# Optimization experiments

Measured on AMD Instinct MI355X. Metric: run time of the kernel, lower is better.

Reference implementation:

```python
import jax, jax.numpy as jnp
import numpy as np

C = 256
D = C // 8  # 32


def setup_inputs() -> dict:
    key = jax.random.key(0)
    ks = jax.random.split(key, 9)
    B, H, W = 4, 64, 64
    x = jax.random.normal(ks[0], (B, C, H, W), dtype=jnp.float32)
    # 1x1 conv weights stored as [out, in] matrices (kernel_size=1)
    s = 1.0 / np.sqrt(C)
    Wf = jax.random.uniform(ks[1], (D, C), jnp.float32, -s, s)
    Wg = jax.random.uniform(ks[2], (D, C), jnp.float32, -s, s)
    Wh = jax.random.uniform(ks[3], (D, C), jnp.float32, -s, s)
    sv = 1.0 / np.sqrt(D)
    Wv = jax.random.uniform(ks[4], (C, D), jnp.float32, -sv, sv)
    bf = jnp.zeros((D,), jnp.float32)
    bg = jnp.zeros((D,), jnp.float32)
    bh = jnp.zeros((D,), jnp.float32)
    bv = jax.random.uniform(ks[5], (C,), jnp.float32, -sv, sv)
    # gamma initialized to zero in the module; use a nonzero value so output is non-trivial
    gamma = jnp.array([0.5], jnp.float32)
    return {"x": x, "Wf": Wf, "bf": bf, "Wg": Wg, "bg": bg,
            "Wh": Wh, "bh": bh, "Wv": Wv, "bv": bv, "gamma": gamma}


def reference(x, Wf, bf, Wg, bg, Wh, bh, Wv, bv, gamma):
    B, Cc, Hh, Ww = x.shape
    N = Hh * Ww
    xf = x.reshape(B, Cc, N)  # flatten spatial tokens, [B, C, N]
    # 1x1 convs == channel matmuls
    f = jnp.einsum('dc,bcn->bdn', Wf, xf) + bf[None, :, None]  # [B, D, N]
    g = jnp.einsum('dc,bcn->bdn', Wg, xf) + bg[None, :, None]
    h = jnp.einsum('dc,bcn->bdn', Wh, xf) + bh[None, :, None]
    # unscaled attention: f^T g -> [B, N, N], softmax over last axis
    attn = jax.nn.softmax(jnp.einsum('bdn,bdm->bnm', f, g), axis=-1)
    # h @ attn: out[:, d, m] = sum_n h[:, d, n] * attn[:, n, m]
    sa = jnp.einsum('bdn,bnm->bdm', h, attn)  # [B, D, N]
    # output 1x1 conv D -> C
    o = jnp.einsum('cd,bdn->bcn', Wv, sa) + bv[None, :, None]
    out = gamma[0] * o.reshape(B, Cc, Hh, Ww)
    return out
```

## Files before the change

### kernel.cpp

```cpp
#include <hip/hip_runtime.h>

typedef __bf16 bf16;
typedef bf16 bf16x4 __attribute__((ext_vector_type(4)));
typedef bf16 bf16x8 __attribute__((ext_vector_type(8)));
typedef float f32x4 __attribute__((ext_vector_type(4)));

#define NB 4
#define NC 256
#define ND 32
#define NN 4096
#define NSPLIT 8
#define MSPLIT 8
#define CSPL 8

__global__ __launch_bounds__(256) void k_wcvt(
    const float* __restrict__ Wf, const float* __restrict__ Wg,
    const float* __restrict__ Wh, bf16* __restrict__ Wstk)
{
    int e0 = (blockIdx.x * 256 + threadIdx.x) * 8;
    int row = e0 >> 8;
    int tensor = row >> 5;
    const float* src = tensor == 0 ? Wf : tensor == 1 ? Wg : Wh;
    const float* sp = src + (row & 31) * NC + (e0 & 255);
    bf16x8 v;
    #pragma unroll
    for (int j = 0; j < 8; ++j) v[j] = (bf16)sp[j];
    *reinterpret_cast<bf16x8*>(Wstk + e0) = v;
}

__global__ __launch_bounds__(512) void k_fgh(
    const float* __restrict__ x,
    const bf16* __restrict__ Wstk,
    const float* __restrict__ bfp, const float* __restrict__ bgp,
    const float* __restrict__ bhp,
    bf16* __restrict__ fT, bf16* __restrict__ gT, bf16* __restrict__ hM)
{
    __shared__ __align__(16) char xb[64 * 512];
    const int b  = blockIdx.y;
    const int n0 = blockIdx.x * 64;
    const int t  = threadIdx.x;
    const int lane = t & 63;
    const int w  = t >> 6;
    const int l15 = lane & 15;
    const int l4  = lane >> 4;

    {
        const int nl  = t & 63;
        const int swz = (nl & 7) << 4;
        const int chi = (t >> 6) * 8;
        #pragma unroll
        for (int pass = 0; pass < 4; ++pass) {
            int c0 = pass * 64 + chi;
            const float* xp = x + ((size_t)b * NC + c0) * NN + n0 + nl;
            bf16x8 v;
            #pragma unroll
            for (int j = 0; j < 8; ++j) v[j] = (bf16)xp[(size_t)j * NN];
            *reinterpret_cast<bf16x8*>(&xb[nl * 512 + ((c0 * 2) ^ swz)]) = v;
        }
    }
    __syncthreads();

    const int ncol = (w & 3) * 16 + l15;
    const int nswz = (ncol & 7) << 4;
    const int n    = n0 + ncol;
    const int dsub = l4 * 4;
    const int rtb  = (w >> 2) * 3;

    #pragma unroll
    for (int rr = 0; rr < 3; ++rr) {
        int rt = rtb + rr;
        int tensor = rt >> 1;
        int d0 = (rt & 1) * 16;
        f32x4 acc = {0.f, 0.f, 0.f, 0.f};
        #pragma unroll
        for (int kc = 0; kc < 8; ++kc) {
            bf16x8 a = *reinterpret_cast<const bf16x8*>(
                Wstk + (rt * 16 + l15) * NC + kc * 32 + l4 * 8);
            bf16x8 bb = *reinterpret_cast<const bf16x8*>(
                &xb[ncol * 512 + ((kc * 64 + l4 * 16) ^ nswz)]);
            acc = __builtin_amdgcn_mfma_f32_16x16x32_bf16(a, bb, acc, 0, 0, 0);
        }
        const float* bsel = tensor == 0 ? bfp : tensor == 1 ? bgp : bhp;
        int dbase = d0 + dsub;
        if (tensor < 2) {
            bf16x4 vv;
            #pragma unroll
            for (int r = 0; r < 4; ++r) vv[r] = (bf16)(acc[r] + bsel[dbase + r]);
            bf16* dst = (tensor == 0 ? fT : gT) + ((size_t)b * NN + n) * ND + dbase;
            *reinterpret_cast<bf16x4*>(dst) = vv;
        } else {
            #pragma unroll
            for (int r = 0; r < 4; ++r)
                hM[((size_t)b * ND + dbase + r) * NN + n] =
                    (bf16)(acc[r] + bsel[dbase + r]);
        }
    }
}

__global__ __launch_bounds__(256) void k_rowsum(
    const bf16* __restrict__ fT, const bf16* __restrict__ gT,
    float* __restrict__ Lpart)
{
    const int b  = blockIdx.z;
    const int ms = blockIdx.y;
    const int nb = blockIdx.x * 64;
    const int t  = threadIdx.x;
    const int lane = t & 63;
    const int w  = t >> 6;
    const int l15 = lane & 15;
    const int l4  = lane >> 4;

    bf16x8 a = *reinterpret_cast<const bf16x8*>(
        fT + ((size_t)b * NN + nb + w * 16 + l15) * ND + l4 * 8);
    float sum0 = 0.f, sum1 = 0.f, sum2 = 0.f, sum3 = 0.f;
    const bf16* gp = gT + (size_t)b * NN * ND
                   + ((size_t)ms * (NN / MSPLIT) + l15) * ND + l4 * 8;
    #pragma unroll 4
    for (int m = 0; m < NN / MSPLIT; m += 32) {
        bf16x8 b0 = *reinterpret_cast<const bf16x8*>(gp + (size_t)m * ND);
        bf16x8 b1 = *reinterpret_cast<const bf16x8*>(gp + (size_t)(m + 16) * ND);
        f32x4 z = {0.f, 0.f, 0.f, 0.f};
        f32x4 s0 = __builtin_amdgcn_mfma_f32_16x16x32_bf16(a, b0, z, 0, 0, 0);
        f32x4 s1 = __builtin_amdgcn_mfma_f32_16x16x32_bf16(a, b1, z, 0, 0, 0);
        sum0 += __expf(s0[0]) + __expf(s1[0]);
        sum1 += __expf(s0[1]) + __expf(s1[1]);
        sum2 += __expf(s0[2]) + __expf(s1[2]);
        sum3 += __expf(s0[3]) + __expf(s1[3]);
    }
    float sv[4] = {sum0, sum1, sum2, sum3};
    #pragma unroll
    for (int r = 0; r < 4; ++r) {
        float v = sv[r];
        v += __shfl_xor(v, 1);
        v += __shfl_xor(v, 2);
        v += __shfl_xor(v, 4);
        v += __shfl_xor(v, 8);
        sv[r] = v;
    }
    if (l15 == 0) {
        #pragma unroll
        for (int r = 0; r < 4; ++r)
            Lpart[((size_t)ms * NB + b) * NN + nb + w * 16 + l4 * 4 + r] = sv[r];
    }
}

__global__ __launch_bounds__(256) void k_attn(
    const bf16* __restrict__ fT, const bf16* __restrict__ gT,
    const bf16* __restrict__ hM, const float* __restrict__ Lpart,
    float* __restrict__ saWS)
{
    __shared__ __align__(16) char fL[64 * 80];
    __shared__ __align__(16) char hL[32 * 144];
    __shared__ __align__(16) char Pl[4 * 2048];
    __shared__ float rlL[64];

    const int b  = blockIdx.z;
    const int ns = blockIdx.y;
    const int m0 = blockIdx.x * 64;
    const int t  = threadIdx.x;
    const int lane = t & 63;
    const int w  = t >> 6;
    const int l15 = lane & 15;
    const int l4  = lane >> 4;

    bf16x8 gfrag = *reinterpret_cast<const bf16x8*>(
        gT + ((size_t)b * NN + m0 + w * 16 + l15) * ND + l4 * 8);

    f32x4 acc0 = {0.f, 0.f, 0.f, 0.f};
    f32x4 acc1 = {0.f, 0.f, 0.f, 0.f};

    char* Pw = &Pl[w * 2048];
    const int mswz = (l15 & 7) << 4;

    const int s_nl = t >> 2;
    const int s_dl = (t & 3) * 8;
    const int s_d  = t >> 3;
    const int s_ne = (t & 7) * 8;
    const bf16* fsrc = fT + (size_t)b * NN * ND;
    const bf16* hsrc = hM + (size_t)b * ND * NN;

    const int nbeg = ns * (NN / NSPLIT);
    const int nend = nbeg + NN / NSPLIT;

    for (int n1 = nbeg; n1 < nend; n1 += 64) {
        __syncthreads();
        *reinterpret_cast<bf16x8*>(&fL[s_nl * 80 + s_dl * 2]) =
            *reinterpret_cast<const bf16x8*>(fsrc + (size_t)(n1 + s_nl) * ND + s_dl);
        *reinterpret_cast<bf16x8*>(&hL[s_d * 144 + s_ne * 2]) =
            *reinterpret_cast<const bf16x8*>(hsrc + (size_t)s_d * NN + n1 + s_ne);
        if (t < 64) {
            float s = 0.f;
            #pragma unroll
            for (int ms = 0; ms < MSPLIT; ++ms)
                s += Lpart[((size_t)ms * NB + b) * NN + n1 + t];
            rlL[t] = 1.0f / s;
        }
        __syncthreads();

        #pragma unroll
        for (int nt = 0; nt < 4; ++nt) {
            bf16x8 afrag = *reinterpret_cast<const bf16x8*>(
                &fL[(nt * 16 + l15) * 80 + l4 * 16]);
            f32x4 z = {0.f, 0.f, 0.f, 0.f};
            f32x4 s = __builtin_amdgcn_mfma_f32_16x16x32_bf16(afrag, gfrag, z, 0, 0, 0);
            bf16x4 p4;
            #pragma unroll
            for (int r = 0; r < 4; ++r)
                p4[r] = (bf16)(__expf(s[r]) * rlL[nt * 16 + l4 * 4 + r]);
            *reinterpret_cast<bf16x4*>(
                &Pw[l15 * 128 + ((nt * 32 + l4 * 8) ^ mswz)]) = p4;
        }
        #pragma unroll
        for (int kc = 0; kc < 2; ++kc) {
            bf16x8 pb = *reinterpret_cast<const bf16x8*>(
                &Pw[l15 * 128 + ((kc * 64 + l4 * 16) ^ mswz)]);
            bf16x8 h0 = *reinterpret_cast<const bf16x8*>(
                &hL[l15 * 144 + kc * 64 + l4 * 16]);
            acc0 = __builtin_amdgcn_mfma_f32_16x16x32_bf16(h0, pb, acc0, 0, 0, 0);
            bf16x8 h1 = *reinterpret_cast<const bf16x8*>(
                &hL[(16 + l15) * 144 + kc * 64 + l4 * 16]);
            acc1 = __builtin_amdgcn_mfma_f32_16x16x32_bf16(h1, pb, acc1, 0, 0, 0);
        }
    }

    float* sp = saWS + (((size_t)ns * NB + b) * NN + m0 + w * 16 + l15) * ND;
    *reinterpret_cast<f32x4*>(sp + l4 * 4)      = acc0;
    *reinterpret_cast<f32x4*>(sp + 16 + l4 * 4) = acc1;
}

__global__ __launch_bounds__(256) void k_proj(
    const float* __restrict__ saWS,
    const float* __restrict__ Wv, const float* __restrict__ bv,
    const float* __restrict__ gamma, float* __restrict__ out)
{
    __shared__ float sa_s[64 * 33];
    const int b  = blockIdx.z;
    const int c0 = blockIdx.y * (NC / CSPL);
    const int m0 = blockIdx.x * 64;
    const int t  = threadIdx.x;

    #pragma unroll
    for (int p = t; p < 64 * 8; p += 256) {
        int m = p >> 3, dq = (p & 7) * 4;
        float s0 = 0.f, s1 = 0.f, s2 = 0.f, s3 = 0.f;
        #pragma unroll
        for (int s4 = 0; s4 < NSPLIT; ++s4) {
            f32x4 v = *reinterpret_cast<const f32x4*>(
                saWS + (((size_t)s4 * NB + b) * NN + m0 + m) * ND + dq);
            s0 += v[0]; s1 += v[1]; s2 += v[2]; s3 += v[3];
        }
        float* dp = &sa_s[m * 33 + dq];
        dp[0] = s0; dp[1] = s1; dp[2] = s2; dp[3] = s3;
    }
    __syncthreads();

    const int mloc = t & 63;
    const int cg   = t >> 6;
    float sav[32];
    #pragma unroll
    for (int d = 0; d < 32; ++d) sav[d] = sa_s[mloc * 33 + d];
    const float g0 = gamma[0];
    float* op = out + (size_t)b * NC * NN + m0 + mloc;
    #pragma unroll
    for (int i = 0; i < 8; ++i) {
        int c = c0 + cg * 8 + i;
        const float* wp = Wv + c * ND;
        float sum = bv[c];
        #pragma unroll
        for (int d = 0; d < 32; ++d) sum = fmaf(wp[d], sav[d], sum);
        op[(size_t)c * NN] = g0 * sum;
    }
}

extern "C" void kernel_launch(void* const* d_in, const int* in_sizes, int n_in,
                              void* d_out, int out_size, void* d_ws, size_t ws_size,
                              hipStream_t stream)
{
    const float* x   = (const float*)d_in[0];
    const float* Wf  = (const float*)d_in[1];
    const float* bfp = (const float*)d_in[2];
    const float* Wg  = (const float*)d_in[3];
    const float* bgp = (const float*)d_in[4];
    const float* Wh  = (const float*)d_in[5];
    const float* bhp = (const float*)d_in[6];
    const float* Wv  = (const float*)d_in[7];
    const float* bv  = (const float*)d_in[8];
    const float* gm  = (const float*)d_in[9];
    float* out = (float*)d_out;

    char* ws = (char*)d_ws;
    bf16*  Wstk  = (bf16*)ws;
    bf16*  fT    = (bf16*)(ws + 49152);
    bf16*  gT    = (bf16*)(ws + 49152 + (1u << 20));
    bf16*  hM    = (bf16*)(ws + 49152 + (2u << 20));
    float* Lpart = (float*)(ws + 49152 + (3u << 20));
    float* saWS  = (float*)(ws + 49152 + (3u << 20) + (512u << 10));

    k_wcvt  <<<dim3(12),              dim3(256), 0, stream>>>(Wf, Wg, Wh, Wstk);
    k_fgh   <<<dim3(64, NB),          dim3(512), 0, stream>>>(x, Wstk, bfp, bgp, bhp, fT, gT, hM);
    k_rowsum<<<dim3(64, MSPLIT, NB),  dim3(256), 0, stream>>>(fT, gT, Lpart);
    k_attn  <<<dim3(64, NSPLIT, NB),  dim3(256), 0, stream>>>(fT, gT, hM, Lpart, saWS);
    k_proj  <<<dim3(64, CSPL, NB),    dim3(256), 0, stream>>>(saWS, Wv, bv, gm, out);
}
```

Baseline: 157.3 us.

## Fuse all stages into one cooperative persistent kernel with grid syncs

Replaces the five separate launches with one cooperative kernel of 512 blocks that loops over virtual work units. Stages are separated by grid-wide barriers: projection of f/g/h (weights now converted inline), row sums, attention, and output projection. The split factors drop from 8 to 4, so each block does more work per unit and there are fewer partial sums to reduce. This removes launch gaps and the weight-conversion kernel, at the cost of grid.sync overhead and fewer parallel blocks per stage. The old multi-kernel path remains as a fallback if the cooperative launch fails.

```diff
diff --git a/kernel.cpp b/kernel.cpp
--- a/kernel.cpp
+++ b/kernel.cpp
@@ -1,4 +1,7 @@
 #include <hip/hip_runtime.h>
+#include <hip/hip_cooperative_groups.h>
+
+namespace cg = cooperative_groups;
 
 typedef __bf16 bf16;
 typedef bf16 bf16x4 __attribute__((ext_vector_type(4)));
@@ -9,9 +12,268 @@
 #define NC 256
 #define ND 32
 #define NN 4096
-#define NSPLIT 8
-#define MSPLIT 8
-#define CSPL 8
+#define SPL 4
+#define GRID 512
+#define VUNITS 2
+
+__global__ __launch_bounds__(256, 2) void k_mega(
+    const float* __restrict__ x,
+    const float* __restrict__ Wf, const float* __restrict__ bfp,
+    const float* __restrict__ Wg, const float* __restrict__ bgp,
+    const float* __restrict__ Wh, const float* __restrict__ bhp,
+    const float* __restrict__ Wv, const float* __restrict__ bv,
+    const float* __restrict__ gamma,
+    bf16* __restrict__ fT, bf16* __restrict__ gT, bf16* __restrict__ hM,
+    float* __restrict__ Lpart, float* __restrict__ saWS,
+    float* __restrict__ out)
+{
+    __shared__ __align__(16) char smem[18432];
+    cg::grid_group grid = cg::this_grid();
+
+    const int bid  = blockIdx.x;
+    const int t    = threadIdx.x;
+    const int lane = t & 63;
+    const int w    = t >> 6;
+    const int l15  = lane & 15;
+    const int l4   = lane >> 4;
+
+    for (int u = 0; u < VUNITS; ++u) {
+        __syncthreads();
+        const int vbid = (u << 9) | bid;
+        const int b    = vbid >> 8;
+        const int rest = vbid & 255;
+        const int n0   = (rest >> 1) * 32;
+        const int half = rest & 1;
+        char* xb = smem;
+
+        {
+            const int nl  = t & 31;
+            const int swz = (nl & 7) << 4;
+            const int chi = (t >> 5) * 8;
+            #pragma unroll
+            for (int pass = 0; pass < 4; ++pass) {
+                int c0 = pass * 64 + chi;
+                const float* xp = x + ((size_t)b * NC + c0) * NN + n0 + nl;
+                bf16x8 v;
+                #pragma unroll
+                for (int j = 0; j < 8; ++j) v[j] = (bf16)xp[(size_t)j * NN];
+                *reinterpret_cast<bf16x8*>(&xb[nl * 512 + ((c0 * 2) ^ swz)]) = v;
+            }
+        }
+        __syncthreads();
+
+        #pragma unroll
+        for (int rep = 0; rep < 2; ++rep) {
+            int tk = w + 4 * rep;
+            if (tk < 6) {
+                const int strip  = tk & 1;
+                const int rt     = half * 3 + (tk >> 1);
+                const int tensor = rt >> 1;
+                const float* Wsel = tensor == 0 ? Wf : tensor == 1 ? Wg : Wh;
+                const float* bsel = tensor == 0 ? bfp : tensor == 1 ? bgp : bhp;
+                const int drow = (rt & 1) * 16 + l15;
+                const int ncol = strip * 16 + l15;
+                const int nswz = (ncol & 7) << 4;
+                f32x4 acc = {0.f, 0.f, 0.f, 0.f};
+                #pragma unroll
+                for (int kc = 0; kc < 8; ++kc) {
+                    const float* wp = Wsel + drow * NC + kc * 32 + l4 * 8;
+                    f32x4 wlo = *reinterpret_cast<const f32x4*>(wp);
+                    f32x4 whi = *reinterpret_cast<const f32x4*>(wp + 4);
+                    bf16x8 a;
+                    #pragma unroll
+                    for (int j = 0; j < 4; ++j) {
+                        a[j]     = (bf16)wlo[j];
+                        a[4 + j] = (bf16)whi[j];
+                    }
+                    bf16x8 bb = *reinterpret_cast<const bf16x8*>(
+                        &xb[ncol * 512 + ((kc * 64 + l4 * 16) ^ nswz)]);
+                    acc = __builtin_amdgcn_mfma_f32_16x16x32_bf16(a, bb, acc, 0, 0, 0);
+                }
+                const int dbase = (rt & 1) * 16 + l4 * 4;
+                const int n = n0 + ncol;
+                if (tensor < 2) {
+                    bf16x4 vv;
+                    #pragma unroll
+                    for (int r = 0; r < 4; ++r) vv[r] = (bf16)(acc[r] + bsel[dbase + r]);
+                    bf16* dst = (tensor == 0 ? fT : gT) + ((size_t)b * NN + n) * ND + dbase;
+                    *reinterpret_cast<bf16x4*>(dst) = vv;
+                } else {
+                    #pragma unroll
+                    for (int r = 0; r < 4; ++r)
+                        hM[((size_t)b * ND + dbase + r) * NN + n] =
+                            (bf16)(acc[r] + bsel[dbase + r]);
+                }
+            }
+        }
+    }
+    __threadfence();
+    grid.sync();
+
+    for (int u = 0; u < VUNITS; ++u) {
+        const int vbid = (u << 9) | bid;
+        const int b  = vbid >> 8;
+        const int r_ = vbid & 255;
+        const int nb = (r_ >> 2) * 64;
+        const int ms = r_ & 3;
+
+        bf16x8 a = *reinterpret_cast<const bf16x8*>(
+            fT + ((size_t)b * NN + nb + w * 16 + l15) * ND + l4 * 8);
+        float sum0 = 0.f, sum1 = 0.f, sum2 = 0.f, sum3 = 0.f;
+        const bf16* gp = gT + (size_t)b * NN * ND
+                       + ((size_t)ms * (NN / SPL) + l15) * ND + l4 * 8;
+        #pragma unroll 4
+        for (int m = 0; m < NN / SPL; m += 32) {
+            bf16x8 b0 = *reinterpret_cast<const bf16x8*>(gp + (size_t)m * ND);
+            bf16x8 b1 = *reinterpret_cast<const bf16x8*>(gp + (size_t)(m + 16) * ND);
+            f32x4 z = {0.f, 0.f, 0.f, 0.f};
+            f32x4 s0 = __builtin_amdgcn_mfma_f32_16x16x32_bf16(a, b0, z, 0, 0, 0);
+            f32x4 s1 = __builtin_amdgcn_mfma_f32_16x16x32_bf16(a, b1, z, 0, 0, 0);
+            sum0 += __expf(s0[0]) + __expf(s1[0]);
+            sum1 += __expf(s0[1]) + __expf(s1[1]);
+            sum2 += __expf(s0[2]) + __expf(s1[2]);
+            sum3 += __expf(s0[3]) + __expf(s1[3]);
+        }
+        float sv[4] = {sum0, sum1, sum2, sum3};
+        #pragma unroll
+        for (int r = 0; r < 4; ++r) {
+            float v = sv[r];
+            v += __shfl_xor(v, 1);
+            v += __shfl_xor(v, 2);
+            v += __shfl_xor(v, 4);
+            v += __shfl_xor(v, 8);
+            sv[r] = v;
+        }
+        if (l15 == 0) {
+            #pragma unroll
+            for (int r = 0; r < 4; ++r)
+                Lpart[((size_t)ms * NB + b) * NN + nb + w * 16 + l4 * 4 + r] = sv[r];
+        }
+    }
+    __threadfence();
+    grid.sync();
+
+    for (int u = 0; u < VUNITS; ++u) {
+        char* fL  = smem;
+        char* hL  = smem + 5120;
+        char* Pl  = smem + 9728;
+        float* rlL = (float*)(smem + 17920);
+
+        const int vbid = (u << 9) | bid;
+        const int b  = vbid >> 8;
+        const int r_ = vbid & 255;
+        const int m0 = (r_ >> 2) * 64;
+        const int ns = r_ & 3;
+
+        bf16x8 gfrag = *reinterpret_cast<const bf16x8*>(
+            gT + ((size_t)b * NN + m0 + w * 16 + l15) * ND + l4 * 8);
+
+        f32x4 acc0 = {0.f, 0.f, 0.f, 0.f};
+        f32x4 acc1 = {0.f, 0.f, 0.f, 0.f};
+
+        char* Pw = &Pl[w * 2048];
+        const int mswz = (l15 & 7) << 4;
+
+        const int s_nl = t >> 2;
+        const int s_dl = (t & 3) * 8;
+        const int s_d  = t >> 3;
+        const int s_ne = (t & 7) * 8;
+        const bf16* fsrc = fT + (size_t)b * NN * ND;
+        const bf16* hsrc = hM + (size_t)b * ND * NN;
+
+        const int nbeg = ns * (NN / SPL);
+        const int nend = nbeg + NN / SPL;
+
+        for (int n1 = nbeg; n1 < nend; n1 += 64) {
+            __syncthreads();
+            *reinterpret_cast<bf16x8*>(&fL[s_nl * 80 + s_dl * 2]) =
+                *reinterpret_cast<const bf16x8*>(fsrc + (size_t)(n1 + s_nl) * ND + s_dl);
+            *reinterpret_cast<bf16x8*>(&hL[s_d * 144 + s_ne * 2]) =
+                *reinterpret_cast<const bf16x8*>(hsrc + (size_t)s_d * NN + n1 + s_ne);
+            if (t < 64) {
+                float s = 0.f;
+                #pragma unroll
+                for (int ms = 0; ms < SPL; ++ms)
+                    s += Lpart[((size_t)ms * NB + b) * NN + n1 + t];
+                rlL[t] = 1.0f / s;
+            }
+            __syncthreads();
+
+            #pragma unroll
+            for (int nt = 0; nt < 4; ++nt) {
+                bf16x8 afrag = *reinterpret_cast<const bf16x8*>(
+                    &fL[(nt * 16 + l15) * 80 + l4 * 16]);
+                f32x4 z = {0.f, 0.f, 0.f, 0.f};
+                f32x4 s = __builtin_amdgcn_mfma_f32_16x16x32_bf16(afrag, gfrag, z, 0, 0, 0);
+                bf16x4 p4;
+                #pragma unroll
+                for (int r = 0; r < 4; ++r)
+                    p4[r] = (bf16)(__expf(s[r]) * rlL[nt * 16 + l4 * 4 + r]);
+                *reinterpret_cast<bf16x4*>(
+                    &Pw[l15 * 128 + ((nt * 32 + l4 * 8) ^ mswz)]) = p4;
+            }
+            #pragma unroll
+            for (int kc = 0; kc < 2; ++kc) {
+                bf16x8 pb = *reinterpret_cast<const bf16x8*>(
+                    &Pw[l15 * 128 + ((kc * 64 + l4 * 16) ^ mswz)]);
+                bf16x8 h0 = *reinterpret_cast<const bf16x8*>(
+                    &hL[l15 * 144 + kc * 64 + l4 * 16]);
+                acc0 = __builtin_amdgcn_mfma_f32_16x16x32_bf16(h0, pb, acc0, 0, 0, 0);
+                bf16x8 h1 = *reinterpret_cast<const bf16x8*>(
+                    &hL[(16 + l15) * 144 + kc * 64 + l4 * 16]);
+                acc1 = __builtin_amdgcn_mfma_f32_16x16x32_bf16(h1, pb, acc1, 0, 0, 0);
+            }
+        }
+
+        float* sp = saWS + (((size_t)ns * NB + b) * NN + m0 + w * 16 + l15) * ND;
+        *reinterpret_cast<f32x4*>(sp + l4 * 4)      = acc0;
+        *reinterpret_cast<f32x4*>(sp + 16 + l4 * 4) = acc1;
+    }
+    __threadfence();
+    grid.sync();
+
+    for (int u = 0; u < VUNITS; ++u) {
+        __syncthreads();
+        float* sa_s = (float*)smem;
+        const int vbid = (u << 9) | bid;
+        const int b  = vbid >> 8;
+        const int r_ = vbid & 255;
+        const int m0 = (r_ >> 2) * 64;
+        const int c0 = (r_ & 3) * 64;
+
+        #pragma unroll
+        for (int p = t; p < 64 * 8; p += 256) {
+            int m = p >> 3, dq = (p & 7) * 4;
+            float s0 = 0.f, s1 = 0.f, s2 = 0.f, s3 = 0.f;
+            #pragma unroll
+            for (int s4 = 0; s4 < SPL; ++s4) {
+                f32x4 v = *reinterpret_cast<const f32x4*>(
+                    saWS + (((size_t)s4 * NB + b) * NN + m0 + m) * ND + dq);
+                s0 += v[0]; s1 += v[1]; s2 += v[2]; s3 += v[3];
+            }
+            float* dp = &sa_s[m * 33 + dq];
+            dp[0] = s0; dp[1] = s1; dp[2] = s2; dp[3] = s3;
+        }
+        __syncthreads();
+
+        const int mloc = t & 63;
+        const int cg_  = t >> 6;
+        float sav[32];
+        #pragma unroll
+        for (int d = 0; d < 32; ++d) sav[d] = sa_s[mloc * 33 + d];
+        const float g0 = gamma[0];
+        float* op = out + (size_t)b * NC * NN + m0 + mloc;
+        #pragma unroll
+        for (int i = 0; i < 16; ++i) {
+            int c = c0 + cg_ * 16 + i;
+            const float* wp = Wv + c * ND;
+            float sum = bv[c];
+            #pragma unroll
+            for (int d = 0; d < 32; ++d) sum = fmaf(wp[d], sav[d], sum);
+            op[(size_t)c * NN] = g0 * sum;
+        }
+    }
+}
 
 __global__ __launch_bounds__(256) void k_wcvt(
     const float* __restrict__ Wf, const float* __restrict__ Wg,
@@ -29,8 +291,7 @@
 }
 
 __global__ __launch_bounds__(512) void k_fgh(
-    const float* __restrict__ x,
-    const bf16* __restrict__ Wstk,
+    const float* __restrict__ x, const bf16* __restrict__ Wstk,
     const float* __restrict__ bfp, const float* __restrict__ bgp,
     const float* __restrict__ bhp,
     bf16* __restrict__ fT, bf16* __restrict__ gT, bf16* __restrict__ hM)
@@ -43,7 +304,6 @@
     const int w  = t >> 6;
     const int l15 = lane & 15;
     const int l4  = lane >> 4;
-
     {
         const int nl  = t & 63;
         const int swz = (nl & 7) << 4;
@@ -59,13 +319,11 @@
         }
     }
     __syncthreads();
-
     const int ncol = (w & 3) * 16 + l15;
     const int nswz = (ncol & 7) << 4;
     const int n    = n0 + ncol;
     const int dsub = l4 * 4;
     const int rtb  = (w >> 2) * 3;
-
     #pragma unroll
     for (int rr = 0; rr < 3; ++rr) {
         int rt = rtb + rr;
@@ -109,14 +367,13 @@
     const int w  = t >> 6;
     const int l15 = lane & 15;
     const int l4  = lane >> 4;
-
     bf16x8 a = *reinterpret_cast<const bf16x8*>(
         fT + ((size_t)b * NN + nb + w * 16 + l15) * ND + l4 * 8);
     float sum0 = 0.f, sum1 = 0.f, sum2 = 0.f, sum3 = 0.f;
     const bf16* gp = gT + (size_t)b * NN * ND
-                   + ((size_t)ms * (NN / MSPLIT) + l15) * ND + l4 * 8;
+                   + ((size_t)ms * (NN / SPL) + l15) * ND + l4 * 8;
     #pragma unroll 4
-    for (int m = 0; m < NN / MSPLIT; m += 32) {
+    for (int m = 0; m < NN / SPL; m += 32) {
         bf16x8 b0 = *reinterpret_cast<const bf16x8*>(gp + (size_t)m * ND);
         bf16x8 b1 = *reinterpret_cast<const bf16x8*>(gp + (size_t)(m + 16) * ND);
         f32x4 z = {0.f, 0.f, 0.f, 0.f};
@@ -153,7 +410,6 @@
     __shared__ __align__(16) char hL[32 * 144];
     __shared__ __align__(16) char Pl[4 * 2048];
     __shared__ float rlL[64];
-
     const int b  = blockIdx.z;
     const int ns = blockIdx.y;
     const int m0 = blockIdx.x * 64;
@@ -162,26 +418,20 @@
     const int w  = t >> 6;
     const int l15 = lane & 15;
     const int l4  = lane >> 4;
-
     bf16x8 gfrag = *reinterpret_cast<const bf16x8*>(
         gT + ((size_t)b * NN + m0 + w * 16 + l15) * ND + l4 * 8);
-
     f32x4 acc0 = {0.f, 0.f, 0.f, 0.f};
     f32x4 acc1 = {0.f, 0.f, 0.f, 0.f};
-
     char* Pw = &Pl[w * 2048];
     const int mswz = (l15 & 7) << 4;
-
     const int s_nl = t >> 2;
     const int s_dl = (t & 3) * 8;
     const int s_d  = t >> 3;
     const int s_ne = (t & 7) * 8;
     const bf16* fsrc = fT + (size_t)b * NN * ND;
     const bf16* hsrc = hM + (size_t)b * ND * NN;
-
-    const int nbeg = ns * (NN / NSPLIT);
-    const int nend = nbeg + NN / NSPLIT;
-
+    const int nbeg = ns * (NN / SPL);
+    const int nend = nbeg + NN / SPL;
     for (int n1 = nbeg; n1 < nend; n1 += 64) {
         __syncthreads();
         *reinterpret_cast<bf16x8*>(&fL[s_nl * 80 + s_dl * 2]) =
@@ -191,12 +441,11 @@
         if (t < 64) {
             float s = 0.f;
             #pragma unroll
-            for (int ms = 0; ms < MSPLIT; ++ms)
+            for (int ms = 0; ms < SPL; ++ms)
                 s += Lpart[((size_t)ms * NB + b) * NN + n1 + t];
             rlL[t] = 1.0f / s;
         }
         __syncthreads();
-
         #pragma unroll
         for (int nt = 0; nt < 4; ++nt) {
             bf16x8 afrag = *reinterpret_cast<const bf16x8*>(
@@ -222,7 +471,6 @@
             acc1 = __builtin_amdgcn_mfma_f32_16x16x32_bf16(h1, pb, acc1, 0, 0, 0);
         }
     }
-
     float* sp = saWS + (((size_t)ns * NB + b) * NN + m0 + w * 16 + l15) * ND;
     *reinterpret_cast<f32x4*>(sp + l4 * 4)      = acc0;
     *reinterpret_cast<f32x4*>(sp + 16 + l4 * 4) = acc1;
@@ -235,16 +483,15 @@
 {
     __shared__ float sa_s[64 * 33];
     const int b  = blockIdx.z;
-    const int c0 = blockIdx.y * (NC / CSPL);
+    const int c0 = blockIdx.y * 64;
     const int m0 = blockIdx.x * 64;
     const int t  = threadIdx.x;
-
     #pragma unroll
     for (int p = t; p < 64 * 8; p += 256) {
         int m = p >> 3, dq = (p & 7) * 4;
         float s0 = 0.f, s1 = 0.f, s2 = 0.f, s3 = 0.f;
         #pragma unroll
-        for (int s4 = 0; s4 < NSPLIT; ++s4) {
+        for (int s4 = 0; s4 < SPL; ++s4) {
             f32x4 v = *reinterpret_cast<const f32x4*>(
                 saWS + (((size_t)s4 * NB + b) * NN + m0 + m) * ND + dq);
             s0 += v[0]; s1 += v[1]; s2 += v[2]; s3 += v[3];
@@ -253,17 +500,16 @@
         dp[0] = s0; dp[1] = s1; dp[2] = s2; dp[3] = s3;
     }
     __syncthreads();
-
     const int mloc = t & 63;
-    const int cg   = t >> 6;
+    const int cg_  = t >> 6;
     float sav[32];
     #pragma unroll
     for (int d = 0; d < 32; ++d) sav[d] = sa_s[mloc * 33 + d];
     const float g0 = gamma[0];
     float* op = out + (size_t)b * NC * NN + m0 + mloc;
     #pragma unroll
-    for (int i = 0; i < 8; ++i) {
-        int c = c0 + cg * 8 + i;
+    for (int i = 0; i < 16; ++i) {
+        int c = c0 + cg_ * 16 + i;
         const float* wp = Wv + c * ND;
         float sum = bv[c];
         #pragma unroll
@@ -286,7 +532,7 @@
     const float* Wv  = (const float*)d_in[7];
     const float* bv  = (const float*)d_in[8];
     const float* gm  = (const float*)d_in[9];
-    float* out = (float*)d_out;
+    float* outp = (float*)d_out;
 
     char* ws = (char*)d_ws;
     bf16*  Wstk  = (bf16*)ws;
@@ -294,11 +540,23 @@
     bf16*  gT    = (bf16*)(ws + 49152 + (1u << 20));
     bf16*  hM    = (bf16*)(ws + 49152 + (2u << 20));
     float* Lpart = (float*)(ws + 49152 + (3u << 20));
-    float* saWS  = (float*)(ws + 49152 + (3u << 20) + (512u << 10));
-
-    k_wcvt  <<<dim3(12),              dim3(256), 0, stream>>>(Wf, Wg, Wh, Wstk);
-    k_fgh   <<<dim3(64, NB),          dim3(512), 0, stream>>>(x, Wstk, bfp, bgp, bhp, fT, gT, hM);
-    k_rowsum<<<dim3(64, MSPLIT, NB),  dim3(256), 0, stream>>>(fT, gT, Lpart);
-    k_attn  <<<dim3(64, NSPLIT, NB),  dim3(256), 0, stream>>>(fT, gT, hM, Lpart, saWS);
-    k_proj  <<<dim3(64, CSPL, NB),    dim3(256), 0, stream>>>(saWS, Wv, bv, gm, out);
-}
+    float* saWS  = (float*)(ws + 49152 + (3u << 20) + (256u << 10));
+
+    void* args[] = {
+        (void*)&x, (void*)&Wf, (void*)&bfp, (void*)&Wg, (void*)&bgp,
+        (void*)&Wh, (void*)&bhp, (void*)&Wv, (void*)&bv, (void*)&gm,
+        (void*)&fT, (void*)&gT, (void*)&hM, (void*)&Lpart, (void*)&saWS,
+        (void*)&outp
+    };
+    hipError_t cerr = hipLaunchCooperativeKernel((const void*)k_mega,
+                                                 dim3(GRID), dim3(256),
+                                                 args, 0, stream);
+    if (cerr != hipSuccess) {
+        (void)hipGetLastError();
+        k_wcvt  <<<dim3(12),            dim3(256), 0, stream>>>(Wf, Wg, Wh, Wstk);
+        k_fgh   <<<dim3(64, NB),        dim3(512), 0, stream>>>(x, Wstk, bfp, bgp, bhp, fT, gT, hM);
+        k_rowsum<<<dim3(64, SPL, NB),   dim3(256), 0, stream>>>(fT, gT, Lpart);
+        k_attn  <<<dim3(64, SPL, NB),   dim3(256), 0, stream>>>(fT, gT, hM, Lpart, saWS);
+        k_proj  <<<dim3(64, 4, NB),     dim3(256), 0, stream>>>(saWS, Wv, bv, gm, outp);
+    }
+}
```

Result: slower. 581.2 us (+269.4%).

## Fuse attention with output projection and fold weight conversion into projection kernel

Applied to the files above, without the earlier changes.

Merges the attention kernel and the output projection into one kernel. Each block now owns 16 query columns, and its four waves split the key range. The partial results are reduced through shared memory instead of a split-N workspace, which removes the saWS round trip and one launch. The weight-conversion kernel is dropped: the fgh kernel reads fp32 weights and converts them inline, and it uses smaller 32-column tiles to launch more blocks. The attention loop now reads f and h fragments straight from global memory instead of staging them in LDS. That removes syncthreads but relies on cache hits, and each block walks the full N range serially with fewer blocks in flight.

```diff
diff --git a/kernel.cpp b/kernel.cpp
--- a/kernel.cpp
+++ b/kernel.cpp
@@ -9,45 +9,30 @@
 #define NC 256
 #define ND 32
 #define NN 4096
-#define NSPLIT 8
 #define MSPLIT 8
-#define CSPL 8
-
-__global__ __launch_bounds__(256) void k_wcvt(
-    const float* __restrict__ Wf, const float* __restrict__ Wg,
-    const float* __restrict__ Wh, bf16* __restrict__ Wstk)
-{
-    int e0 = (blockIdx.x * 256 + threadIdx.x) * 8;
-    int row = e0 >> 8;
-    int tensor = row >> 5;
-    const float* src = tensor == 0 ? Wf : tensor == 1 ? Wg : Wh;
-    const float* sp = src + (row & 31) * NC + (e0 & 255);
-    bf16x8 v;
-    #pragma unroll
-    for (int j = 0; j < 8; ++j) v[j] = (bf16)sp[j];
-    *reinterpret_cast<bf16x8*>(Wstk + e0) = v;
-}
-
-__global__ __launch_bounds__(512) void k_fgh(
+
+__global__ __launch_bounds__(256, 4) void k_fgh(
     const float* __restrict__ x,
-    const bf16* __restrict__ Wstk,
-    const float* __restrict__ bfp, const float* __restrict__ bgp,
-    const float* __restrict__ bhp,
+    const float* __restrict__ Wf, const float* __restrict__ bfp,
+    const float* __restrict__ Wg, const float* __restrict__ bgp,
+    const float* __restrict__ Wh, const float* __restrict__ bhp,
     bf16* __restrict__ fT, bf16* __restrict__ gT, bf16* __restrict__ hM)
 {
-    __shared__ __align__(16) char xb[64 * 512];
-    const int b  = blockIdx.y;
-    const int n0 = blockIdx.x * 64;
-    const int t  = threadIdx.x;
+    __shared__ __align__(16) char xb[32 * 512];
+    const int b    = blockIdx.y;
+    const int rest = blockIdx.x;
+    const int n0   = (rest >> 1) * 32;
+    const int half = rest & 1;
+    const int t    = threadIdx.x;
     const int lane = t & 63;
-    const int w  = t >> 6;
-    const int l15 = lane & 15;
-    const int l4  = lane >> 4;
+    const int w    = t >> 6;
+    const int l15  = lane & 15;
+    const int l4   = lane >> 4;
 
     {
-        const int nl  = t & 63;
+        const int nl  = t & 31;
         const int swz = (nl & 7) << 4;
-        const int chi = (t >> 6) * 8;
+        const int chi = (t >> 5) * 8;
         #pragma unroll
         for (int pass = 0; pass < 4; ++pass) {
             int c0 = pass * 64 + chi;
@@ -60,39 +45,48 @@
     }
     __syncthreads();
 
-    const int ncol = (w & 3) * 16 + l15;
-    const int nswz = (ncol & 7) << 4;
-    const int n    = n0 + ncol;
-    const int dsub = l4 * 4;
-    const int rtb  = (w >> 2) * 3;
-
-    #pragma unroll
-    for (int rr = 0; rr < 3; ++rr) {
-        int rt = rtb + rr;
-        int tensor = rt >> 1;
-        int d0 = (rt & 1) * 16;
-        f32x4 acc = {0.f, 0.f, 0.f, 0.f};
-        #pragma unroll
-        for (int kc = 0; kc < 8; ++kc) {
-            bf16x8 a = *reinterpret_cast<const bf16x8*>(
-                Wstk + (rt * 16 + l15) * NC + kc * 32 + l4 * 8);
-            bf16x8 bb = *reinterpret_cast<const bf16x8*>(
-                &xb[ncol * 512 + ((kc * 64 + l4 * 16) ^ nswz)]);
-            acc = __builtin_amdgcn_mfma_f32_16x16x32_bf16(a, bb, acc, 0, 0, 0);
-        }
-        const float* bsel = tensor == 0 ? bfp : tensor == 1 ? bgp : bhp;
-        int dbase = d0 + dsub;
-        if (tensor < 2) {
-            bf16x4 vv;
+    #pragma unroll
+    for (int rep = 0; rep < 2; ++rep) {
+        int tk = w + 4 * rep;
+        if (tk < 6) {
+            const int strip  = tk & 1;
+            const int rt     = half * 3 + (tk >> 1);
+            const int tensor = rt >> 1;
+            const float* Wsel = tensor == 0 ? Wf : tensor == 1 ? Wg : Wh;
+            const float* bsel = tensor == 0 ? bfp : tensor == 1 ? bgp : bhp;
+            const int drow = (rt & 1) * 16 + l15;
+            const int ncol = strip * 16 + l15;
+            const int nswz = (ncol & 7) << 4;
+            f32x4 acc = {0.f, 0.f, 0.f, 0.f};
             #pragma unroll
-            for (int r = 0; r < 4; ++r) vv[r] = (bf16)(acc[r] + bsel[dbase + r]);
-            bf16* dst = (tensor == 0 ? fT : gT) + ((size_t)b * NN + n) * ND + dbase;
-            *reinterpret_cast<bf16x4*>(dst) = vv;
-        } else {
-            #pragma unroll
-            for (int r = 0; r < 4; ++r)
-                hM[((size_t)b * ND + dbase + r) * NN + n] =
-                    (bf16)(acc[r] + bsel[dbase + r]);
+            for (int kc = 0; kc < 8; ++kc) {
+                const float* wp = Wsel + drow * NC + kc * 32 + l4 * 8;
+                f32x4 wlo = *reinterpret_cast<const f32x4*>(wp);
+                f32x4 whi = *reinterpret_cast<const f32x4*>(wp + 4);
+                bf16x8 a;
+                #pragma unroll
+                for (int j = 0; j < 4; ++j) {
+                    a[j]     = (bf16)wlo[j];
+                    a[4 + j] = (bf16)whi[j];
+                }
+                bf16x8 bb = *reinterpret_cast<const bf16x8*>(
+                    &xb[ncol * 512 + ((kc * 64 + l4 * 16) ^ nswz)]);
+                acc = __builtin_amdgcn_mfma_f32_16x16x32_bf16(a, bb, acc, 0, 0, 0);
+            }
+            const int dbase = (rt & 1) * 16 + l4 * 4;
+            const int n = n0 + ncol;
+            if (tensor < 2) {
+                bf16x4 vv;
+                #pragma unroll
+                for (int r = 0; r < 4; ++r) vv[r] = (bf16)(acc[r] + bsel[dbase + r]);
+                bf16* dst = (tensor == 0 ? fT : gT) + ((size_t)b * NN + n) * ND + dbase;
+                *reinterpret_cast<bf16x4*>(dst) = vv;
+            } else {
+                #pragma unroll
+                for (int r = 0; r < 4; ++r)
+                    hM[((size_t)b * ND + dbase + r) * NN + n] =
+                        (bf16)(acc[r] + bsel[dbase + r]);
+            }
         }
     }
 }
@@ -144,19 +138,18 @@
     }
 }
 
-__global__ __launch_bounds__(256) void k_attn(
+__global__ __launch_bounds__(256, 4) void k_attnproj(
     const bf16* __restrict__ fT, const bf16* __restrict__ gT,
     const bf16* __restrict__ hM, const float* __restrict__ Lpart,
-    float* __restrict__ saWS)
-{
-    __shared__ __align__(16) char fL[64 * 80];
-    __shared__ __align__(16) char hL[32 * 144];
+    const float* __restrict__ Wv, const float* __restrict__ bv,
+    const float* __restrict__ gamma, float* __restrict__ out)
+{
     __shared__ __align__(16) char Pl[4 * 2048];
-    __shared__ float rlL[64];
-
-    const int b  = blockIdx.z;
-    const int ns = blockIdx.y;
-    const int m0 = blockIdx.x * 64;
+    __shared__ float rlw[4][64];
+    __shared__ float sa_s[4][32 * 16];
+
+    const int b  = blockIdx.y;
+    const int m0 = blockIdx.x * 16;
     const int t  = threadIdx.x;
     const int lane = t & 63;
     const int w  = t >> 6;
@@ -164,49 +157,35 @@
     const int l4  = lane >> 4;
 
     bf16x8 gfrag = *reinterpret_cast<const bf16x8*>(
-        gT + ((size_t)b * NN + m0 + w * 16 + l15) * ND + l4 * 8);
+        gT + ((size_t)b * NN + m0 + l15) * ND + l4 * 8);
 
     f32x4 acc0 = {0.f, 0.f, 0.f, 0.f};
     f32x4 acc1 = {0.f, 0.f, 0.f, 0.f};
 
     char* Pw = &Pl[w * 2048];
     const int mswz = (l15 & 7) << 4;
-
-    const int s_nl = t >> 2;
-    const int s_dl = (t & 3) * 8;
-    const int s_d  = t >> 3;
-    const int s_ne = (t & 7) * 8;
     const bf16* fsrc = fT + (size_t)b * NN * ND;
     const bf16* hsrc = hM + (size_t)b * ND * NN;
 
-    const int nbeg = ns * (NN / NSPLIT);
-    const int nend = nbeg + NN / NSPLIT;
-
-    for (int n1 = nbeg; n1 < nend; n1 += 64) {
-        __syncthreads();
-        *reinterpret_cast<bf16x8*>(&fL[s_nl * 80 + s_dl * 2]) =
-            *reinterpret_cast<const bf16x8*>(fsrc + (size_t)(n1 + s_nl) * ND + s_dl);
-        *reinterpret_cast<bf16x8*>(&hL[s_d * 144 + s_ne * 2]) =
-            *reinterpret_cast<const bf16x8*>(hsrc + (size_t)s_d * NN + n1 + s_ne);
-        if (t < 64) {
-            float s = 0.f;
-            #pragma unroll
-            for (int ms = 0; ms < MSPLIT; ++ms)
-                s += Lpart[((size_t)ms * NB + b) * NN + n1 + t];
-            rlL[t] = 1.0f / s;
-        }
-        __syncthreads();
+    for (int it = 0; it < 16; ++it) {
+        const int n1 = it * 256 + w * 64;
+
+        float s = 0.f;
+        #pragma unroll
+        for (int ms = 0; ms < MSPLIT; ++ms)
+            s += Lpart[((size_t)ms * NB + b) * NN + n1 + lane];
+        rlw[w][lane] = 1.0f / s;
 
         #pragma unroll
         for (int nt = 0; nt < 4; ++nt) {
             bf16x8 afrag = *reinterpret_cast<const bf16x8*>(
-                &fL[(nt * 16 + l15) * 80 + l4 * 16]);
+                fsrc + (size_t)(n1 + nt * 16 + l15) * ND + l4 * 8);
             f32x4 z = {0.f, 0.f, 0.f, 0.f};
-            f32x4 s = __builtin_amdgcn_mfma_f32_16x16x32_bf16(afrag, gfrag, z, 0, 0, 0);
+            f32x4 sv = __builtin_amdgcn_mfma_f32_16x16x32_bf16(afrag, gfrag, z, 0, 0, 0);
             bf16x4 p4;
             #pragma unroll
             for (int r = 0; r < 4; ++r)
-                p4[r] = (bf16)(__expf(s[r]) * rlL[nt * 16 + l4 * 4 + r]);
+                p4[r] = (bf16)(__expf(sv[r]) * rlw[w][nt * 16 + l4 * 4 + r]);
             *reinterpret_cast<bf16x4*>(
                 &Pw[l15 * 128 + ((nt * 32 + l4 * 8) ^ mswz)]) = p4;
         }
@@ -215,55 +194,33 @@
             bf16x8 pb = *reinterpret_cast<const bf16x8*>(
                 &Pw[l15 * 128 + ((kc * 64 + l4 * 16) ^ mswz)]);
             bf16x8 h0 = *reinterpret_cast<const bf16x8*>(
-                &hL[l15 * 144 + kc * 64 + l4 * 16]);
+                hsrc + (size_t)l15 * NN + n1 + kc * 32 + l4 * 8);
             acc0 = __builtin_amdgcn_mfma_f32_16x16x32_bf16(h0, pb, acc0, 0, 0, 0);
             bf16x8 h1 = *reinterpret_cast<const bf16x8*>(
-                &hL[(16 + l15) * 144 + kc * 64 + l4 * 16]);
+                hsrc + (size_t)(16 + l15) * NN + n1 + kc * 32 + l4 * 8);
             acc1 = __builtin_amdgcn_mfma_f32_16x16x32_bf16(h1, pb, acc1, 0, 0, 0);
         }
     }
 
-    float* sp = saWS + (((size_t)ns * NB + b) * NN + m0 + w * 16 + l15) * ND;
-    *reinterpret_cast<f32x4*>(sp + l4 * 4)      = acc0;
-    *reinterpret_cast<f32x4*>(sp + 16 + l4 * 4) = acc1;
-}
-
-__global__ __launch_bounds__(256) void k_proj(
-    const float* __restrict__ saWS,
-    const float* __restrict__ Wv, const float* __restrict__ bv,
-    const float* __restrict__ gamma, float* __restrict__ out)
-{
-    __shared__ float sa_s[64 * 33];
-    const int b  = blockIdx.z;
-    const int c0 = blockIdx.y * (NC / CSPL);
-    const int m0 = blockIdx.x * 64;
-    const int t  = threadIdx.x;
-
-    #pragma unroll
-    for (int p = t; p < 64 * 8; p += 256) {
-        int m = p >> 3, dq = (p & 7) * 4;
-        float s0 = 0.f, s1 = 0.f, s2 = 0.f, s3 = 0.f;
-        #pragma unroll
-        for (int s4 = 0; s4 < NSPLIT; ++s4) {
-            f32x4 v = *reinterpret_cast<const f32x4*>(
-                saWS + (((size_t)s4 * NB + b) * NN + m0 + m) * ND + dq);
-            s0 += v[0]; s1 += v[1]; s2 += v[2]; s3 += v[3];
-        }
-        float* dp = &sa_s[m * 33 + dq];
-        dp[0] = s0; dp[1] = s1; dp[2] = s2; dp[3] = s3;
+    #pragma unroll
+    for (int r = 0; r < 4; ++r) {
+        sa_s[w][(l4 * 4 + r) * 16 + l15]        = acc0[r];
+        sa_s[w][(16 + l4 * 4 + r) * 16 + l15]   = acc1[r];
     }
     __syncthreads();
 
-    const int mloc = t & 63;
-    const int cg   = t >> 6;
+    const int m  = t & 15;
+    const int cb = (t >> 4) * 16;
     float sav[32];
     #pragma unroll
-    for (int d = 0; d < 32; ++d) sav[d] = sa_s[mloc * 33 + d];
+    for (int d = 0; d < 32; ++d)
+        sav[d] = sa_s[0][d * 16 + m] + sa_s[1][d * 16 + m]
+               + sa_s[2][d * 16 + m] + sa_s[3][d * 16 + m];
     const float g0 = gamma[0];
-    float* op = out + (size_t)b * NC * NN + m0 + mloc;
-    #pragma unroll
-    for (int i = 0; i < 8; ++i) {
-        int c = c0 + cg * 8 + i;
+    float* op = out + (size_t)b * NC * NN + m0 + m;
+    #pragma unroll
+    for (int i = 0; i < 16; ++i) {
+        int c = cb + i;
         const float* wp = Wv + c * ND;
         float sum = bv[c];
         #pragma unroll
@@ -286,19 +243,17 @@
     const float* Wv  = (const float*)d_in[7];
     const float* bv  = (const float*)d_in[8];
     const float* gm  = (const float*)d_in[9];
-    float* out = (float*)d_out;
+    float* outp = (float*)d_out;
 
     char* ws = (char*)d_ws;
-    bf16*  Wstk  = (bf16*)ws;
-    bf16*  fT    = (bf16*)(ws + 49152);
-    bf16*  gT    = (bf16*)(ws + 49152 + (1u << 20));
-    bf16*  hM    = (bf16*)(ws + 49152 + (2u << 20));
-    float* Lpart = (float*)(ws + 49152 + (3u << 20));
-    float* saWS  = (float*)(ws + 49152 + (3u << 20) + (512u << 10));
-
-    k_wcvt  <<<dim3(12),              dim3(256), 0, stream>>>(Wf, Wg, Wh, Wstk);
-    k_fgh   <<<dim3(64, NB),          dim3(512), 0, stream>>>(x, Wstk, bfp, bgp, bhp, fT, gT, hM);
-    k_rowsum<<<dim3(64, MSPLIT, NB),  dim3(256), 0, stream>>>(fT, gT, Lpart);
-    k_attn  <<<dim3(64, NSPLIT, NB),  dim3(256), 0, stream>>>(fT, gT, hM, Lpart, saWS);
-    k_proj  <<<dim3(64, CSPL, NB),    dim3(256), 0, stream>>>(saWS, Wv, bv, gm, out);
-}
+    bf16*  fT    = (bf16*)ws;
+    bf16*  gT    = (bf16*)(ws + (1u << 20));
+    bf16*  hM    = (bf16*)(ws + (2u << 20));
+    float* Lpart = (float*)(ws + (3u << 20));
+
+    k_fgh     <<<dim3(256, NB),        dim3(256), 0, stream>>>(
+        x, Wf, bfp, Wg, bgp, Wh, bhp, fT, gT, hM);
+    k_rowsum  <<<dim3(64, MSPLIT, NB), dim3(256), 0, stream>>>(fT, gT, Lpart);
+    k_attnproj<<<dim3(256, NB),        dim3(256), 0, stream>>>(
+        fT, gT, hM, Lpart, Wv, bv, gm, outp);
+}
```

Result: slower. 179.3 us (+14.0%).
